# Kernel tuning notes

Measured on AMD Instinct MI355X. Metric: run time of the kernel, lower is better.

## Reference

```python
import jax, jax.numpy as jnp
import numpy as np

N = 50000          # nodes
E = 800000         # directed edges (avg degree 16)
D_IN = 128
H1, H2, H3 = 128, 128, 64


def setup_inputs() -> dict:
    key = jax.random.key(0)
    ks = jax.random.split(key, 12)
    s = 0.05  # small init scale
    return {
        "x": jax.random.normal(ks[0], (N, D_IN), dtype=jnp.float32),
        "edge_index": jax.random.randint(ks[1], (2, E), 0, N, dtype=jnp.int32),
        "W1": jax.random.normal(ks[2], (D_IN, H1), dtype=jnp.float32) * s,
        "b1": jnp.zeros((H1,), jnp.float32),
        "W2": jax.random.normal(ks[3], (H1, H2), dtype=jnp.float32) * s,
        "b2": jnp.zeros((H2,), jnp.float32),
        "W3": jax.random.normal(ks[4], (H2, H3), dtype=jnp.float32) * s,
        "b3": jnp.zeros((H3,), jnp.float32),
        "attn_W": jax.random.normal(ks[5], (H3, 1), dtype=jnp.float32) * s,
        "attn_b": jnp.zeros((1,), jnp.float32),
        "fc_W": jax.random.normal(ks[6], (H3, 1), dtype=jnp.float32) * s,
        "fc_b": jnp.zeros((1,), jnp.float32),
    }


def reference(x, edge_index, W1, b1, W2, b2, W3, b3, attn_W, attn_b, fc_W, fc_b):
    n = x.shape[0]
    self_loop = jnp.arange(n, dtype=edge_index.dtype)
    src = jnp.concatenate([edge_index[0], self_loop])  # [E+N]
    dst = jnp.concatenate([edge_index[1], self_loop])
    # GCN symmetric normalization with self-loops: deg over dst (col)
    deg = jax.ops.segment_sum(jnp.ones_like(dst, jnp.float32), dst, num_segments=n)
    dis = jax.lax.rsqrt(deg)  # deg >= 1 because of self-loops
    norm = dis[src] * dis[dst]  # [E+N]

    def gcn_conv(h, W, b):
        h = h @ W                                   # [N, out]
        msg = h[src] * norm[:, None]                # gather + scale
        out = jax.ops.segment_sum(msg, dst, num_segments=n)  # scatter-add
        return out + b

    h = jax.nn.relu(gcn_conv(x, W1, b1))
    # dropout: inference mode -> identity
    h = jax.nn.relu(gcn_conv(h, W2, b2))
    h = jax.nn.relu(gcn_conv(h, W3, b3))

    attn = jax.nn.softmax(h @ attn_W + attn_b, axis=0)  # softmax over node dim, [N,1]
    h = h * attn
    out = jax.nn.sigmoid(h @ fc_W + fc_b)  # [N,1]
    return out, attn
```

## Files before the change

kernel.cpp:

```cpp
#include <hip/hip_runtime.h>
#include <math.h>


typedef __attribute__((ext_vector_type(8))) short bf16x8;
typedef __attribute__((ext_vector_type(4))) float f32x4;

__device__ inline float bf2f(unsigned short u) {
  return __uint_as_float(((unsigned int)u) << 16);
}
__device__ inline unsigned short f2bf(float f) {
  unsigned int x = __float_as_uint(f);
  return (unsigned short)((x + 0x7FFFu + ((x >> 16) & 1u)) >> 16);
}
__device__ inline unsigned char f2fp8(float f) {
  int p = __builtin_amdgcn_cvt_pk_fp8_f32(f, f, 0, false);
  return (unsigned char)(p & 0xFF);
}

__global__ __launch_bounds__(256) void prep_kernel(int* __restrict__ counts,
    int* __restrict__ cursor, int n, const float* __restrict__ W1,
    const float* __restrict__ W2, const float* __restrict__ W3,
    unsigned short* __restrict__ Wt1, unsigned short* __restrict__ Wt2,
    unsigned short* __restrict__ Wt3) {
  int i = blockIdx.x * 256 + threadIdx.x;
  if (i < n) { counts[i] = 0; cursor[i] = 0; }
  if (i < 16384) {
    Wt1[(i & 127) * 128 + (i >> 7)] = f2bf(W1[i]);
  } else if (i < 32768) {
    int j = i - 16384;
    Wt2[(j & 127) * 128 + (j >> 7)] = f2bf(W2[j]);
  } else if (i < 40960) {
    int j = i - 32768;
    Wt3[(j & 63) * 128 + (j >> 6)] = f2bf(W3[j]);
  }
}

__global__ __launch_bounds__(256) void count_kernel(const int* __restrict__ dst,
                                                    int* __restrict__ counts, int E) {
  int e = blockIdx.x * blockDim.x + threadIdx.x;
  if (e < E) atomicAdd(&counts[dst[e]], 1);
}

__global__ __launch_bounds__(256) void block_sum_kernel(const int* __restrict__ counts,
                                                        int* __restrict__ bsums, int n) {
  int i = blockIdx.x * 256 + threadIdx.x;
  int v = (i < n) ? counts[i] : 0;
#pragma unroll
  for (int o = 32; o > 0; o >>= 1) v += __shfl_xor(v, o);
  __shared__ int w[4];
  if ((threadIdx.x & 63) == 0) w[threadIdx.x >> 6] = v;
  __syncthreads();
  if (threadIdx.x == 0) bsums[blockIdx.x] = w[0] + w[1] + w[2] + w[3];
}

__global__ __launch_bounds__(256) void block_scan_kernel(const int* __restrict__ bsums,
    int* __restrict__ bprefix, int* __restrict__ offsets, int nb, int n) {
  __shared__ int lds[256];
  int v = (threadIdx.x < (unsigned)nb) ? bsums[threadIdx.x] : 0;
  lds[threadIdx.x] = v;
  __syncthreads();
  for (int off = 1; off < 256; off <<= 1) {
    int t = (threadIdx.x >= (unsigned)off) ? lds[threadIdx.x - off] : 0;
    __syncthreads();
    lds[threadIdx.x] += t;
    __syncthreads();
  }
  if (threadIdx.x < (unsigned)nb) bprefix[threadIdx.x] = lds[threadIdx.x] - v;
  if (threadIdx.x == 255) offsets[n] = lds[255];
}

__global__ __launch_bounds__(256) void scan_apply_kernel(const int* __restrict__ counts,
    const int* __restrict__ bprefix, int* __restrict__ offsets,
    float* __restrict__ dis, int n) {
  __shared__ int lds[256];
  int i = blockIdx.x * 256 + threadIdx.x;
  int v = (i < n) ? counts[i] : 0;
  lds[threadIdx.x] = v;
  __syncthreads();
  for (int off = 1; off < 256; off <<= 1) {
    int t = (threadIdx.x >= (unsigned)off) ? lds[threadIdx.x - off] : 0;
    __syncthreads();
    lds[threadIdx.x] += t;
    __syncthreads();
  }
  if (i < n) {
    offsets[i] = bprefix[blockIdx.x] + lds[threadIdx.x] - v;
    dis[i] = rsqrtf((float)v + 1.0f);
  }
}

__global__ __launch_bounds__(256) void fill_kernel(const int* __restrict__ src,
    const int* __restrict__ dst, const int* __restrict__ offsets, int* __restrict__ cursor,
    const float* __restrict__ dis, unsigned int* __restrict__ csr, int E) {
  int e = blockIdx.x * blockDim.x + threadIdx.x;
  if (e >= E) return;
  int d = dst[e], s = src[e];
  int pos = offsets[d] + atomicAdd(&cursor[d], 1);
  csr[pos] = (unsigned int)s | ((unsigned int)f2bf(dis[s] * dis[d]) << 16);
}

template <int OUT, bool AF32>
__global__ __launch_bounds__(256) void gemm_mfma_kernel(const void* __restrict__ Ap,
    const unsigned short* __restrict__ Wt, unsigned char* __restrict__ T, int nrows) {
  constexpr int NC = OUT / 16;
  int wave = threadIdx.x >> 6;
  int lane = threadIdx.x & 63;
  int r15  = lane & 15;
  int kgrp = lane >> 4;
  int base = blockIdx.x * 64 + wave * 16;
  int row  = base + r15;

  f32x4 acc[NC];
#pragma unroll
  for (int c = 0; c < NC; c++) acc[c] = {0.f, 0.f, 0.f, 0.f};

#pragma unroll
  for (int kk = 0; kk < 4; kk++) {
    int k0 = kk * 32 + kgrp * 8;
    bf16x8 a = {0, 0, 0, 0, 0, 0, 0, 0};
    if (row < nrows) {
      if (AF32) {
        const float* A = (const float*)Ap;
        float4 lo = *(const float4*)(A + (size_t)row * 128 + k0);
        float4 hi = *(const float4*)(A + (size_t)row * 128 + k0 + 4);
        a[0] = (short)f2bf(lo.x); a[1] = (short)f2bf(lo.y);
        a[2] = (short)f2bf(lo.z); a[3] = (short)f2bf(lo.w);
        a[4] = (short)f2bf(hi.x); a[5] = (short)f2bf(hi.y);
        a[6] = (short)f2bf(hi.z); a[7] = (short)f2bf(hi.w);
      } else {
        const unsigned short* A = (const unsigned short*)Ap;
        a = *(const bf16x8*)(A + (size_t)row * 128 + k0);
      }
    }
#pragma unroll
    for (int c = 0; c < NC; c++) {
      bf16x8 b = *(const bf16x8*)(Wt + (size_t)(c * 16 + r15) * 128 + k0);
      acc[c] = __builtin_amdgcn_mfma_f32_16x16x32_bf16(a, b, acc[c], 0, 0, 0);
    }
  }

  int orow0 = base + kgrp * 4;
#pragma unroll
  for (int c = 0; c < NC; c++) {
#pragma unroll
    for (int j = 0; j < 4; j++) {
      int r = orow0 + j;
      if (r < nrows)
        T[(size_t)r * OUT + c * 16 + r15] = f2fp8(acc[c][j] * 16.f);
    }
  }
}

__global__ __launch_bounds__(256) void aggregate128_kernel(
    const unsigned char* __restrict__ T, const int* __restrict__ offsets,
    const unsigned int* __restrict__ csr, const float* __restrict__ dis,
    const float* __restrict__ bias, unsigned short* __restrict__ H, int n) {
  int node = (blockIdx.x * blockDim.x + threadIdx.x) >> 6;
  int lane = threadIdx.x & 63;
  if (node >= n) return;

  float di = dis[node];
  float sn = di * di;
  int beg = offsets[node], end = offsets[node + 1];

  unsigned int tv = *(const unsigned short*)(T + (size_t)node * 128 + lane * 2);
  float acc0 = __builtin_amdgcn_cvt_f32_fp8(tv, 0) * sn;
  float acc1 = __builtin_amdgcn_cvt_f32_fp8(tv, 1) * sn;

  int e = beg;
  for (; e + 8 <= end; e += 8) {
    uint4 q0 = *(const uint4*)(csr + e);
    uint4 q1 = *(const uint4*)(csr + e + 4);
    unsigned int t0 = *(const unsigned short*)(T + (size_t)(q0.x & 0xFFFF) * 128 + lane * 2);
    unsigned int t1 = *(const unsigned short*)(T + (size_t)(q0.y & 0xFFFF) * 128 + lane * 2);
    unsigned int t2 = *(const unsigned short*)(T + (size_t)(q0.z & 0xFFFF) * 128 + lane * 2);
    unsigned int t3 = *(const unsigned short*)(T + (size_t)(q0.w & 0xFFFF) * 128 + lane * 2);
    unsigned int t4 = *(const unsigned short*)(T + (size_t)(q1.x & 0xFFFF) * 128 + lane * 2);
    unsigned int t5 = *(const unsigned short*)(T + (size_t)(q1.y & 0xFFFF) * 128 + lane * 2);
    unsigned int t6 = *(const unsigned short*)(T + (size_t)(q1.z & 0xFFFF) * 128 + lane * 2);
    unsigned int t7 = *(const unsigned short*)(T + (size_t)(q1.w & 0xFFFF) * 128 + lane * 2);
    float n0 = bf2f((unsigned short)(q0.x >> 16));
    float n1 = bf2f((unsigned short)(q0.y >> 16));
    float n2 = bf2f((unsigned short)(q0.z >> 16));
    float n3 = bf2f((unsigned short)(q0.w >> 16));
    float n4 = bf2f((unsigned short)(q1.x >> 16));
    float n5 = bf2f((unsigned short)(q1.y >> 16));
    float n6 = bf2f((unsigned short)(q1.z >> 16));
    float n7 = bf2f((unsigned short)(q1.w >> 16));
    acc0 = fmaf(__builtin_amdgcn_cvt_f32_fp8(t0, 0), n0, acc0);
    acc1 = fmaf(__builtin_amdgcn_cvt_f32_fp8(t0, 1), n0, acc1);
    acc0 = fmaf(__builtin_amdgcn_cvt_f32_fp8(t1, 0), n1, acc0);
    acc1 = fmaf(__builtin_amdgcn_cvt_f32_fp8(t1, 1), n1, acc1);
    acc0 = fmaf(__builtin_amdgcn_cvt_f32_fp8(t2, 0), n2, acc0);
    acc1 = fmaf(__builtin_amdgcn_cvt_f32_fp8(t2, 1), n2, acc1);
    acc0 = fmaf(__builtin_amdgcn_cvt_f32_fp8(t3, 0), n3, acc0);
    acc1 = fmaf(__builtin_amdgcn_cvt_f32_fp8(t3, 1), n3, acc1);
    acc0 = fmaf(__builtin_amdgcn_cvt_f32_fp8(t4, 0), n4, acc0);
    acc1 = fmaf(__builtin_amdgcn_cvt_f32_fp8(t4, 1), n4, acc1);
    acc0 = fmaf(__builtin_amdgcn_cvt_f32_fp8(t5, 0), n5, acc0);
    acc1 = fmaf(__builtin_amdgcn_cvt_f32_fp8(t5, 1), n5, acc1);
    acc0 = fmaf(__builtin_amdgcn_cvt_f32_fp8(t6, 0), n6, acc0);
    acc1 = fmaf(__builtin_amdgcn_cvt_f32_fp8(t6, 1), n6, acc1);
    acc0 = fmaf(__builtin_amdgcn_cvt_f32_fp8(t7, 0), n7, acc0);
    acc1 = fmaf(__builtin_amdgcn_cvt_f32_fp8(t7, 1), n7, acc1);
  }
  for (; e < end; e++) {
    unsigned int c = csr[e];
    unsigned int tv2 = *(const unsigned short*)(T + (size_t)(c & 0xFFFF) * 128 + lane * 2);
    float nr = bf2f((unsigned short)(c >> 16));
    acc0 = fmaf(__builtin_amdgcn_cvt_f32_fp8(tv2, 0), nr, acc0);
    acc1 = fmaf(__builtin_amdgcn_cvt_f32_fp8(tv2, 1), nr, acc1);
  }
  float h0 = acc0 * 0.0625f + bias[lane * 2];
  float h1 = acc1 * 0.0625f + bias[lane * 2 + 1];
  ushort2 o;
  o.x = f2bf(h0 > 0.f ? h0 : 0.f);
  o.y = f2bf(h1 > 0.f ? h1 : 0.f);
  *(ushort2*)(H + (size_t)node * 128 + lane * 2) = o;
}

__global__ __launch_bounds__(256) void agg3_dots_kernel(
    const unsigned char* __restrict__ T, const int* __restrict__ offsets,
    const unsigned int* __restrict__ csr, const float* __restrict__ dis,
    const float* __restrict__ bias, const float* __restrict__ attn_W,
    const float* __restrict__ attn_b, const float* __restrict__ fc_W,
    float* __restrict__ logits, float* __restrict__ fdot, int n) {
  int node = (blockIdx.x * blockDim.x + threadIdx.x) >> 6;
  int lane = threadIdx.x & 63;
  if (node >= n) return;

  float di = dis[node];
  float sn = di * di;
  int beg = offsets[node], end = offsets[node + 1];

  unsigned int tv = T[(size_t)node * 64 + lane];
  float acc = __builtin_amdgcn_cvt_f32_fp8(tv, 0) * sn;

  int e = beg;
  for (; e + 8 <= end; e += 8) {
    uint4 q0 = *(const uint4*)(csr + e);
    uint4 q1 = *(const uint4*)(csr + e + 4);
    unsigned int t0 = T[(size_t)(q0.x & 0xFFFF) * 64 + lane];
    unsigned int t1 = T[(size_t)(q0.y & 0xFFFF) * 64 + lane];
    unsigned int t2 = T[(size_t)(q0.z & 0xFFFF) * 64 + lane];
    unsigned int t3 = T[(size_t)(q0.w & 0xFFFF) * 64 + lane];
    unsigned int t4 = T[(size_t)(q1.x & 0xFFFF) * 64 + lane];
    unsigned int t5 = T[(size_t)(q1.y & 0xFFFF) * 64 + lane];
    unsigned int t6 = T[(size_t)(q1.z & 0xFFFF) * 64 + lane];
    unsigned int t7 = T[(size_t)(q1.w & 0xFFFF) * 64 + lane];
    acc = fmaf(__builtin_amdgcn_cvt_f32_fp8(t0, 0), bf2f((unsigned short)(q0.x >> 16)), acc);
    acc = fmaf(__builtin_amdgcn_cvt_f32_fp8(t1, 0), bf2f((unsigned short)(q0.y >> 16)), acc);
    acc = fmaf(__builtin_amdgcn_cvt_f32_fp8(t2, 0), bf2f((unsigned short)(q0.z >> 16)), acc);
    acc = fmaf(__builtin_amdgcn_cvt_f32_fp8(t3, 0), bf2f((unsigned short)(q0.w >> 16)), acc);
    acc = fmaf(__builtin_amdgcn_cvt_f32_fp8(t4, 0), bf2f((unsigned short)(q1.x >> 16)), acc);
    acc = fmaf(__builtin_amdgcn_cvt_f32_fp8(t5, 0), bf2f((unsigned short)(q1.y >> 16)), acc);
    acc = fmaf(__builtin_amdgcn_cvt_f32_fp8(t6, 0), bf2f((unsigned short)(q1.z >> 16)), acc);
    acc = fmaf(__builtin_amdgcn_cvt_f32_fp8(t7, 0), bf2f((unsigned short)(q1.w >> 16)), acc);
  }
  for (; e < end; e++) {
    unsigned int c = csr[e];
    unsigned int tv2 = T[(size_t)(c & 0xFFFF) * 64 + lane];
    acc = fmaf(__builtin_amdgcn_cvt_f32_fp8(tv2, 0), bf2f((unsigned short)(c >> 16)), acc);
  }
  float h = acc * 0.0625f + bias[lane];
  h = h > 0.f ? h : 0.f;
  float a = h * attn_W[lane];
  float f = h * fc_W[lane];
#pragma unroll
  for (int m = 32; m > 0; m >>= 1) { a += __shfl_xor(a, m); f += __shfl_xor(f, m); }
  if (lane == 0) { logits[node] = a + attn_b[0]; fdot[node] = f; }
}

__global__ __launch_bounds__(256) void smax_partial_kernel(const float* __restrict__ l,
    float2* __restrict__ part, int n) {
  float m = -3.4e38f, s = 0.f;
  for (int i = blockIdx.x * 256 + threadIdx.x; i < n; i += gridDim.x * 256) {
    float v = l[i];
    float nm = fmaxf(m, v);
    s = s * __expf(m - nm) + __expf(v - nm);
    m = nm;
  }
#pragma unroll
  for (int o = 32; o > 0; o >>= 1) {
    float mo = __shfl_xor(m, o), so = __shfl_xor(s, o);
    float nm = fmaxf(m, mo);
    s = s * __expf(m - nm) + so * __expf(mo - nm);
    m = nm;
  }
  __shared__ float wm[4], ws[4];
  if ((threadIdx.x & 63) == 0) { wm[threadIdx.x >> 6] = m; ws[threadIdx.x >> 6] = s; }
  __syncthreads();
  if (threadIdx.x == 0) {
    float gm = fmaxf(fmaxf(wm[0], wm[1]), fmaxf(wm[2], wm[3]));
    float gs = ws[0] * __expf(wm[0] - gm) + ws[1] * __expf(wm[1] - gm) +
               ws[2] * __expf(wm[2] - gm) + ws[3] * __expf(wm[3] - gm);
    part[blockIdx.x] = make_float2(gm, gs);
  }
}

__global__ __launch_bounds__(64) void smax_combine_kernel(const float2* __restrict__ part,
    float2* __restrict__ gms, int np) {
  int lane = threadIdx.x;
  float m = -3.4e38f, s = 0.f;
  if (lane < np) { float2 p = part[lane]; m = p.x; s = p.y; }
#pragma unroll
  for (int o = 32; o > 0; o >>= 1) {
    float mo = __shfl_xor(m, o), so = __shfl_xor(s, o);
    float nm = fmaxf(m, mo);
    s = s * __expf(m - nm) + so * __expf(mo - nm);
    m = nm;
  }
  if (lane == 0) gms[0] = make_float2(m, s);
}

__global__ __launch_bounds__(256) void out_kernel(const float* __restrict__ l,
    const float2* __restrict__ gms, const float* __restrict__ fdot,
    const float* __restrict__ fc_b, float* __restrict__ out, int n) {
  int i = blockIdx.x * blockDim.x + threadIdx.x;
  if (i >= n) return;
  float2 g = gms[0];
  float attn = __expf(l[i] - g.x) / g.y;
  float z = fdot[i] * attn + fc_b[0];
  out[i]     = 1.f / (1.f + __expf(-z));
  out[n + i] = attn;
}

extern "C" void kernel_launch(void* const* d_in, const int* in_sizes, int n_in,
                              void* d_out, int out_size, void* d_ws, size_t ws_size,
                              hipStream_t stream) {
  const float* x      = (const float*)d_in[0];
  const int*   ei     = (const int*)d_in[1];
  const float* W1     = (const float*)d_in[2];
  const float* b1     = (const float*)d_in[3];
  const float* W2     = (const float*)d_in[4];
  const float* b2     = (const float*)d_in[5];
  const float* W3     = (const float*)d_in[6];
  const float* b3     = (const float*)d_in[7];
  const float* attn_W = (const float*)d_in[8];
  const float* attn_b = (const float*)d_in[9];
  const float* fc_W   = (const float*)d_in[10];
  const float* fc_b   = (const float*)d_in[11];

  const int N = in_sizes[0] / 128;
  const int E = in_sizes[1] / 2;
  const int NB = (N + 255) / 256;
  const int* src = ei;
  const int* dst = ei + E;

  char* p = (char*)d_ws;
  auto alloc = [&](size_t bytes) {
    void* r = (void*)p;
    p += (bytes + 255) & ~(size_t)255;
    return r;
  };
  int*   counts  = (int*)alloc((size_t)N * 4);
  int*   cursor  = (int*)alloc((size_t)N * 4);
  int*   offsets = (int*)alloc((size_t)(N + 1) * 4);
  float* dis     = (float*)alloc((size_t)N * 4);
  unsigned int*   csr  = (unsigned int*)alloc((size_t)E * 4);
  unsigned char*  tbuf = (unsigned char*)alloc((size_t)N * 128);
  unsigned short* hbuf = (unsigned short*)alloc((size_t)N * 128 * 2);
  unsigned short* wt1  = (unsigned short*)alloc(128 * 128 * 2);
  unsigned short* wt2  = (unsigned short*)alloc(128 * 128 * 2);
  unsigned short* wt3  = (unsigned short*)alloc(64 * 128 * 2);
  float* logits  = (float*)alloc((size_t)N * 4);
  float* fdot    = (float*)alloc((size_t)N * 4);
  int*   bsums   = (int*)alloc(256 * 4);
  int*   bprefix = (int*)alloc(256 * 4);
  float2* part   = (float2*)alloc(64 * 8);
  float2* gms    = (float2*)alloc(256);

  int PB = NB > 160 ? NB : 160;
  prep_kernel<<<PB, 256, 0, stream>>>(counts, cursor, N, W1, W2, W3, wt1, wt2, wt3);
  count_kernel<<<(E + 255) / 256, 256, 0, stream>>>(dst, counts, E);
  block_sum_kernel<<<NB, 256, 0, stream>>>(counts, bsums, N);
  block_scan_kernel<<<1, 256, 0, stream>>>(bsums, bprefix, offsets, NB, N);
  scan_apply_kernel<<<NB, 256, 0, stream>>>(counts, bprefix, offsets, dis, N);
  fill_kernel<<<(E + 255) / 256, 256, 0, stream>>>(src, dst, offsets, cursor, dis, csr, E);

  const int GB = (N + 63) / 64;
  gemm_mfma_kernel<128, true><<<GB, 256, 0, stream>>>(x, wt1, tbuf, N);
  aggregate128_kernel<<<(N + 3) / 4, 256, 0, stream>>>(tbuf, offsets, csr, dis, b1, hbuf, N);
  gemm_mfma_kernel<128, false><<<GB, 256, 0, stream>>>(hbuf, wt2, tbuf, N);
  aggregate128_kernel<<<(N + 3) / 4, 256, 0, stream>>>(tbuf, offsets, csr, dis, b2, hbuf, N);
  gemm_mfma_kernel<64, false><<<GB, 256, 0, stream>>>(hbuf, wt3, tbuf, N);
  agg3_dots_kernel<<<(N + 3) / 4, 256, 0, stream>>>(tbuf, offsets, csr, dis, b3,
                                                    attn_W, attn_b, fc_W, logits, fdot, N);

  smax_partial_kernel<<<64, 256, 0, stream>>>(logits, part, N);
  smax_combine_kernel<<<1, 64, 0, stream>>>(part, gms, 64);
  out_kernel<<<(N + 255) / 256, 256, 0, stream>>>(logits, gms, fdot, fc_b, (float*)d_out, N);
}
```

Baseline: 335.3 us.

## Split neighbor edges across sub-wave groups with 8-byte gathers; double GEMM rows per wave

The aggregation kernels now split each node's wavefront into sub-groups (4 for the 128-wide layers, 8 for the 64-wide layer). Each lane gathers 8 fp8 features with one 8-byte load, and different sub-groups handle different edges concurrently. Partial sums are then combined with cross-lane shuffles. This replaces narrow 1-2 byte per-lane gathers with wider loads and more independent memory requests in flight, at the cost of shuffle reductions and possibly idle sub-groups on low-degree nodes. Separately, the MFMA GEMM now computes 32 rows per wave instead of 16, which reuses each weight fragment load across two MFMAs at the cost of more registers.

After: 301.3 us. 10.2% less time.

```diff
diff --git a/kernel.cpp b/kernel.cpp
--- a/kernel.cpp
+++ b/kernel.cpp
@@ -4,6 +4,7 @@
 
 typedef __attribute__((ext_vector_type(8))) short bf16x8;
 typedef __attribute__((ext_vector_type(4))) float f32x4;
+typedef __attribute__((ext_vector_type(8))) unsigned short u16x8;
 
 __device__ inline float bf2f(unsigned short u) {
   return __uint_as_float(((unsigned int)u) << 16);
@@ -15,6 +16,26 @@
 __device__ inline unsigned char f2fp8(float f) {
   int p = __builtin_amdgcn_cvt_pk_fp8_f32(f, f, 0, false);
   return (unsigned char)(p & 0xFF);
+}
+__device__ inline void fp8x8_scale(uint2 t, float s, float (&acc)[8]) {
+  acc[0] = __builtin_amdgcn_cvt_f32_fp8(t.x, 0) * s;
+  acc[1] = __builtin_amdgcn_cvt_f32_fp8(t.x, 1) * s;
+  acc[2] = __builtin_amdgcn_cvt_f32_fp8(t.x, 2) * s;
+  acc[3] = __builtin_amdgcn_cvt_f32_fp8(t.x, 3) * s;
+  acc[4] = __builtin_amdgcn_cvt_f32_fp8(t.y, 0) * s;
+  acc[5] = __builtin_amdgcn_cvt_f32_fp8(t.y, 1) * s;
+  acc[6] = __builtin_amdgcn_cvt_f32_fp8(t.y, 2) * s;
+  acc[7] = __builtin_amdgcn_cvt_f32_fp8(t.y, 3) * s;
+}
+__device__ inline void fp8x8_fma(uint2 t, float nr, float (&acc)[8]) {
+  acc[0] = fmaf(__builtin_amdgcn_cvt_f32_fp8(t.x, 0), nr, acc[0]);
+  acc[1] = fmaf(__builtin_amdgcn_cvt_f32_fp8(t.x, 1), nr, acc[1]);
+  acc[2] = fmaf(__builtin_amdgcn_cvt_f32_fp8(t.x, 2), nr, acc[2]);
+  acc[3] = fmaf(__builtin_amdgcn_cvt_f32_fp8(t.x, 3), nr, acc[3]);
+  acc[4] = fmaf(__builtin_amdgcn_cvt_f32_fp8(t.y, 0), nr, acc[4]);
+  acc[5] = fmaf(__builtin_amdgcn_cvt_f32_fp8(t.y, 1), nr, acc[5]);
+  acc[6] = fmaf(__builtin_amdgcn_cvt_f32_fp8(t.y, 2), nr, acc[6]);
+  acc[7] = fmaf(__builtin_amdgcn_cvt_f32_fp8(t.y, 3), nr, acc[7]);
 }
 
 __global__ __launch_bounds__(256) void prep_kernel(int* __restrict__ counts,
@@ -107,46 +128,63 @@
   int lane = threadIdx.x & 63;
   int r15  = lane & 15;
   int kgrp = lane >> 4;
-  int base = blockIdx.x * 64 + wave * 16;
-  int row  = base + r15;
-
-  f32x4 acc[NC];
-#pragma unroll
-  for (int c = 0; c < NC; c++) acc[c] = {0.f, 0.f, 0.f, 0.f};
+  int base = blockIdx.x * 128 + wave * 32;
+  int row0 = base + r15;
+  int row1 = base + 16 + r15;
+
+  f32x4 acc[2][NC];
+#pragma unroll
+  for (int r = 0; r < 2; r++)
+#pragma unroll
+    for (int c = 0; c < NC; c++) acc[r][c] = {0.f, 0.f, 0.f, 0.f};
 
 #pragma unroll
   for (int kk = 0; kk < 4; kk++) {
     int k0 = kk * 32 + kgrp * 8;
-    bf16x8 a = {0, 0, 0, 0, 0, 0, 0, 0};
-    if (row < nrows) {
-      if (AF32) {
-        const float* A = (const float*)Ap;
-        float4 lo = *(const float4*)(A + (size_t)row * 128 + k0);
-        float4 hi = *(const float4*)(A + (size_t)row * 128 + k0 + 4);
-        a[0] = (short)f2bf(lo.x); a[1] = (short)f2bf(lo.y);
-        a[2] = (short)f2bf(lo.z); a[3] = (short)f2bf(lo.w);
-        a[4] = (short)f2bf(hi.x); a[5] = (short)f2bf(hi.y);
-        a[6] = (short)f2bf(hi.z); a[7] = (short)f2bf(hi.w);
-      } else {
-        const unsigned short* A = (const unsigned short*)Ap;
-        a = *(const bf16x8*)(A + (size_t)row * 128 + k0);
+    bf16x8 a0 = {0, 0, 0, 0, 0, 0, 0, 0};
+    bf16x8 a1 = {0, 0, 0, 0, 0, 0, 0, 0};
+    if (AF32) {
+      const float* A = (const float*)Ap;
+      if (row0 < nrows) {
+        float4 lo = *(const float4*)(A + (size_t)row0 * 128 + k0);
+        float4 hi = *(const float4*)(A + (size_t)row0 * 128 + k0 + 4);
+        a0[0] = (short)f2bf(lo.x); a0[1] = (short)f2bf(lo.y);
+        a0[2] = (short)f2bf(lo.z); a0[3] = (short)f2bf(lo.w);
+        a0[4] = (short)f2bf(hi.x); a0[5] = (short)f2bf(hi.y);
+        a0[6] = (short)f2bf(hi.z); a0[7] = (short)f2bf(hi.w);
       }
+      if (row1 < nrows) {
+        float4 lo = *(const float4*)(A + (size_t)row1 * 128 + k0);
+        float4 hi = *(const float4*)(A + (size_t)row1 * 128 + k0 + 4);
+        a1[0] = (short)f2bf(lo.x); a1[1] = (short)f2bf(lo.y);
+        a1[2] = (short)f2bf(lo.z); a1[3] = (short)f2bf(lo.w);
+        a1[4] = (short)f2bf(hi.x); a1[5] = (short)f2bf(hi.y);
+        a1[6] = (short)f2bf(hi.z); a1[7] = (short)f2bf(hi.w);
+      }
+    } else {
+      const unsigned short* A = (const unsigned short*)Ap;
+      if (row0 < nrows) a0 = *(const bf16x8*)(A + (size_t)row0 * 128 + k0);
+      if (row1 < nrows) a1 = *(const bf16x8*)(A + (size_t)row1 * 128 + k0);
     }
 #pragma unroll
     for (int c = 0; c < NC; c++) {
       bf16x8 b = *(const bf16x8*)(Wt + (size_t)(c * 16 + r15) * 128 + k0);
-      acc[c] = __builtin_amdgcn_mfma_f32_16x16x32_bf16(a, b, acc[c], 0, 0, 0);
+      acc[0][c] = __builtin_amdgcn_mfma_f32_16x16x32_bf16(a0, b, acc[0][c], 0, 0, 0);
+      acc[1][c] = __builtin_amdgcn_mfma_f32_16x16x32_bf16(a1, b, acc[1][c], 0, 0, 0);
     }
   }
 
-  int orow0 = base + kgrp * 4;
-#pragma unroll
-  for (int c = 0; c < NC; c++) {
-#pragma unroll
-    for (int j = 0; j < 4; j++) {
-      int r = orow0 + j;
-      if (r < nrows)
-        T[(size_t)r * OUT + c * 16 + r15] = f2fp8(acc[c][j] * 16.f);
+#pragma unroll
+  for (int r = 0; r < 2; r++) {
+    int orow0 = base + r * 16 + kgrp * 4;
+#pragma unroll
+    for (int c = 0; c < NC; c++) {
+#pragma unroll
+      for (int j = 0; j < 4; j++) {
+        int rr = orow0 + j;
+        if (rr < nrows)
+          T[(size_t)rr * OUT + c * 16 + r15] = f2fp8(acc[r][c][j] * 16.f);
+      }
     }
   }
 }
@@ -158,65 +196,52 @@
   int node = (blockIdx.x * blockDim.x + threadIdx.x) >> 6;
   int lane = threadIdx.x & 63;
   if (node >= n) return;
+  int sub = lane >> 4;
+  int fl  = lane & 15;
 
   float di = dis[node];
   float sn = di * di;
   int beg = offsets[node], end = offsets[node + 1];
 
-  unsigned int tv = *(const unsigned short*)(T + (size_t)node * 128 + lane * 2);
-  float acc0 = __builtin_amdgcn_cvt_f32_fp8(tv, 0) * sn;
-  float acc1 = __builtin_amdgcn_cvt_f32_fp8(tv, 1) * sn;
-
-  int e = beg;
-  for (; e + 8 <= end; e += 8) {
-    uint4 q0 = *(const uint4*)(csr + e);
-    uint4 q1 = *(const uint4*)(csr + e + 4);
-    unsigned int t0 = *(const unsigned short*)(T + (size_t)(q0.x & 0xFFFF) * 128 + lane * 2);
-    unsigned int t1 = *(const unsigned short*)(T + (size_t)(q0.y & 0xFFFF) * 128 + lane * 2);
-    unsigned int t2 = *(const unsigned short*)(T + (size_t)(q0.z & 0xFFFF) * 128 + lane * 2);
-    unsigned int t3 = *(const unsigned short*)(T + (size_t)(q0.w & 0xFFFF) * 128 + lane * 2);
-    unsigned int t4 = *(const unsigned short*)(T + (size_t)(q1.x & 0xFFFF) * 128 + lane * 2);
-    unsigned int t5 = *(const unsigned short*)(T + (size_t)(q1.y & 0xFFFF) * 128 + lane * 2);
-    unsigned int t6 = *(const unsigned short*)(T + (size_t)(q1.z & 0xFFFF) * 128 + lane * 2);
-    unsigned int t7 = *(const unsigned short*)(T + (size_t)(q1.w & 0xFFFF) * 128 + lane * 2);
-    float n0 = bf2f((unsigned short)(q0.x >> 16));
-    float n1 = bf2f((unsigned short)(q0.y >> 16));
-    float n2 = bf2f((unsigned short)(q0.z >> 16));
-    float n3 = bf2f((unsigned short)(q0.w >> 16));
-    float n4 = bf2f((unsigned short)(q1.x >> 16));
-    float n5 = bf2f((unsigned short)(q1.y >> 16));
-    float n6 = bf2f((unsigned short)(q1.z >> 16));
-    float n7 = bf2f((unsigned short)(q1.w >> 16));
-    acc0 = fmaf(__builtin_amdgcn_cvt_f32_fp8(t0, 0), n0, acc0);
-    acc1 = fmaf(__builtin_amdgcn_cvt_f32_fp8(t0, 1), n0, acc1);
-    acc0 = fmaf(__builtin_amdgcn_cvt_f32_fp8(t1, 0), n1, acc0);
-    acc1 = fmaf(__builtin_amdgcn_cvt_f32_fp8(t1, 1), n1, acc1);
-    acc0 = fmaf(__builtin_amdgcn_cvt_f32_fp8(t2, 0), n2, acc0);
-    acc1 = fmaf(__builtin_amdgcn_cvt_f32_fp8(t2, 1), n2, acc1);
-    acc0 = fmaf(__builtin_amdgcn_cvt_f32_fp8(t3, 0), n3, acc0);
-    acc1 = fmaf(__builtin_amdgcn_cvt_f32_fp8(t3, 1), n3, acc1);
-    acc0 = fmaf(__builtin_amdgcn_cvt_f32_fp8(t4, 0), n4, acc0);
-    acc1 = fmaf(__builtin_amdgcn_cvt_f32_fp8(t4, 1), n4, acc1);
-    acc0 = fmaf(__builtin_amdgcn_cvt_f32_fp8(t5, 0), n5, acc0);
-    acc1 = fmaf(__builtin_amdgcn_cvt_f32_fp8(t5, 1), n5, acc1);
-    acc0 = fmaf(__builtin_amdgcn_cvt_f32_fp8(t6, 0), n6, acc0);
-    acc1 = fmaf(__builtin_amdgcn_cvt_f32_fp8(t6, 1), n6, acc1);
-    acc0 = fmaf(__builtin_amdgcn_cvt_f32_fp8(t7, 0), n7, acc0);
-    acc1 = fmaf(__builtin_amdgcn_cvt_f32_fp8(t7, 1), n7, acc1);
-  }
-  for (; e < end; e++) {
-    unsigned int c = csr[e];
-    unsigned int tv2 = *(const unsigned short*)(T + (size_t)(c & 0xFFFF) * 128 + lane * 2);
-    float nr = bf2f((unsigned short)(c >> 16));
-    acc0 = fmaf(__builtin_amdgcn_cvt_f32_fp8(tv2, 0), nr, acc0);
-    acc1 = fmaf(__builtin_amdgcn_cvt_f32_fp8(tv2, 1), nr, acc1);
-  }
-  float h0 = acc0 * 0.0625f + bias[lane * 2];
-  float h1 = acc1 * 0.0625f + bias[lane * 2 + 1];
-  ushort2 o;
-  o.x = f2bf(h0 > 0.f ? h0 : 0.f);
-  o.y = f2bf(h1 > 0.f ? h1 : 0.f);
-  *(ushort2*)(H + (size_t)node * 128 + lane * 2) = o;
+  float acc[8];
+  {
+    uint2 tv = *(const uint2*)(T + (size_t)node * 128 + fl * 8);
+    fp8x8_scale(tv, (sub == 0) ? sn : 0.f, acc);
+  }
+
+  int e = beg + sub;
+  for (; e + 4 < end; e += 8) {
+    unsigned int c0 = csr[e], c1 = csr[e + 4];
+    uint2 t0 = *(const uint2*)(T + (size_t)(c0 & 0xFFFF) * 128 + fl * 8);
+    uint2 t1 = *(const uint2*)(T + (size_t)(c1 & 0xFFFF) * 128 + fl * 8);
+    fp8x8_fma(t0, bf2f((unsigned short)(c0 >> 16)), acc);
+    fp8x8_fma(t1, bf2f((unsigned short)(c1 >> 16)), acc);
+  }
+  if (e < end) {
+    unsigned int c0 = csr[e];
+    uint2 t0 = *(const uint2*)(T + (size_t)(c0 & 0xFFFF) * 128 + fl * 8);
+    fp8x8_fma(t0, bf2f((unsigned short)(c0 >> 16)), acc);
+  }
+
+#pragma unroll
+  for (int j = 0; j < 8; j++) {
+    acc[j] += __shfl_xor(acc[j], 16);
+    acc[j] += __shfl_xor(acc[j], 32);
+  }
+
+  if (sub == 0) {
+    float4 b0 = *(const float4*)(bias + fl * 8);
+    float4 b1 = *(const float4*)(bias + fl * 8 + 4);
+    float hb[8];
+    hb[0] = acc[0] * 0.0625f + b0.x; hb[1] = acc[1] * 0.0625f + b0.y;
+    hb[2] = acc[2] * 0.0625f + b0.z; hb[3] = acc[3] * 0.0625f + b0.w;
+    hb[4] = acc[4] * 0.0625f + b1.x; hb[5] = acc[5] * 0.0625f + b1.y;
+    hb[6] = acc[6] * 0.0625f + b1.z; hb[7] = acc[7] * 0.0625f + b1.w;
+    u16x8 o;
+#pragma unroll
+    for (int j = 0; j < 8; j++) o[j] = f2bf(hb[j] > 0.f ? hb[j] : 0.f);
+    *(u16x8*)(H + (size_t)node * 128 + fl * 8) = o;
+  }
 }
 
 __global__ __launch_bounds__(256) void agg3_dots_kernel(
@@ -228,46 +253,59 @@
   int node = (blockIdx.x * blockDim.x + threadIdx.x) >> 6;
   int lane = threadIdx.x & 63;
   if (node >= n) return;
+  int sub = lane >> 3;
+  int fl  = lane & 7;
 
   float di = dis[node];
   float sn = di * di;
   int beg = offsets[node], end = offsets[node + 1];
 
-  unsigned int tv = T[(size_t)node * 64 + lane];
-  float acc = __builtin_amdgcn_cvt_f32_fp8(tv, 0) * sn;
-
-  int e = beg;
-  for (; e + 8 <= end; e += 8) {
-    uint4 q0 = *(const uint4*)(csr + e);
-    uint4 q1 = *(const uint4*)(csr + e + 4);
-    unsigned int t0 = T[(size_t)(q0.x & 0xFFFF) * 64 + lane];
-    unsigned int t1 = T[(size_t)(q0.y & 0xFFFF) * 64 + lane];
-    unsigned int t2 = T[(size_t)(q0.z & 0xFFFF) * 64 + lane];
-    unsigned int t3 = T[(size_t)(q0.w & 0xFFFF) * 64 + lane];
-    unsigned int t4 = T[(size_t)(q1.x & 0xFFFF) * 64 + lane];
-    unsigned int t5 = T[(size_t)(q1.y & 0xFFFF) * 64 + lane];
-    unsigned int t6 = T[(size_t)(q1.z & 0xFFFF) * 64 + lane];
-    unsigned int t7 = T[(size_t)(q1.w & 0xFFFF) * 64 + lane];
-    acc = fmaf(__builtin_amdgcn_cvt_f32_fp8(t0, 0), bf2f((unsigned short)(q0.x >> 16)), acc);
-    acc = fmaf(__builtin_amdgcn_cvt_f32_fp8(t1, 0), bf2f((unsigned short)(q0.y >> 16)), acc);
-    acc = fmaf(__builtin_amdgcn_cvt_f32_fp8(t2, 0), bf2f((unsigned short)(q0.z >> 16)), acc);
-    acc = fmaf(__builtin_amdgcn_cvt_f32_fp8(t3, 0), bf2f((unsigned short)(q0.w >> 16)), acc);
-    acc = fmaf(__builtin_amdgcn_cvt_f32_fp8(t4, 0), bf2f((unsigned short)(q1.x >> 16)), acc);
-    acc = fmaf(__builtin_amdgcn_cvt_f32_fp8(t5, 0), bf2f((unsigned short)(q1.y >> 16)), acc);
-    acc = fmaf(__builtin_amdgcn_cvt_f32_fp8(t6, 0), bf2f((unsigned short)(q1.z >> 16)), acc);
-    acc = fmaf(__builtin_amdgcn_cvt_f32_fp8(t7, 0), bf2f((unsigned short)(q1.w >> 16)), acc);
-  }
-  for (; e < end; e++) {
-    unsigned int c = csr[e];
-    unsigned int tv2 = T[(size_t)(c & 0xFFFF) * 64 + lane];
-    acc = fmaf(__builtin_amdgcn_cvt_f32_fp8(tv2, 0), bf2f((unsigned short)(c >> 16)), acc);
-  }
-  float h = acc * 0.0625f + bias[lane];
-  h = h > 0.f ? h : 0.f;
-  float a = h * attn_W[lane];
-  float f = h * fc_W[lane];
-#pragma unroll
-  for (int m = 32; m > 0; m >>= 1) { a += __shfl_xor(a, m); f += __shfl_xor(f, m); }
+  float acc[8];
+  {
+    uint2 tv = *(const uint2*)(T + (size_t)node * 64 + fl * 8);
+    fp8x8_scale(tv, (sub == 0) ? sn : 0.f, acc);
+  }
+
+  int e = beg + sub;
+  for (; e + 8 < end; e += 16) {
+    unsigned int c0 = csr[e], c1 = csr[e + 8];
+    uint2 t0 = *(const uint2*)(T + (size_t)(c0 & 0xFFFF) * 64 + fl * 8);
+    uint2 t1 = *(const uint2*)(T + (size_t)(c1 & 0xFFFF) * 64 + fl * 8);
+    fp8x8_fma(t0, bf2f((unsigned short)(c0 >> 16)), acc);
+    fp8x8_fma(t1, bf2f((unsigned short)(c1 >> 16)), acc);
+  }
+  if (e < end) {
+    unsigned int c0 = csr[e];
+    uint2 t0 = *(const uint2*)(T + (size_t)(c0 & 0xFFFF) * 64 + fl * 8);
+    fp8x8_fma(t0, bf2f((unsigned short)(c0 >> 16)), acc);
+  }
+
+#pragma unroll
+  for (int j = 0; j < 8; j++) {
+    acc[j] += __shfl_xor(acc[j], 8);
+    acc[j] += __shfl_xor(acc[j], 16);
+    acc[j] += __shfl_xor(acc[j], 32);
+  }
+
+  float4 b0 = *(const float4*)(bias + fl * 8);
+  float4 b1 = *(const float4*)(bias + fl * 8 + 4);
+  float4 aw0 = *(const float4*)(attn_W + fl * 8);
+  float4 aw1 = *(const float4*)(attn_W + fl * 8 + 4);
+  float4 fw0 = *(const float4*)(fc_W + fl * 8);
+  float4 fw1 = *(const float4*)(fc_W + fl * 8 + 4);
+  float h[8];
+  h[0] = acc[0] * 0.0625f + b0.x; h[1] = acc[1] * 0.0625f + b0.y;
+  h[2] = acc[2] * 0.0625f + b0.z; h[3] = acc[3] * 0.0625f + b0.w;
+  h[4] = acc[4] * 0.0625f + b1.x; h[5] = acc[5] * 0.0625f + b1.y;
+  h[6] = acc[6] * 0.0625f + b1.z; h[7] = acc[7] * 0.0625f + b1.w;
+#pragma unroll
+  for (int j = 0; j < 8; j++) h[j] = h[j] > 0.f ? h[j] : 0.f;
+  float a = h[0] * aw0.x + h[1] * aw0.y + h[2] * aw0.z + h[3] * aw0.w +
+            h[4] * aw1.x + h[5] * aw1.y + h[6] * aw1.z + h[7] * aw1.w;
+  float f = h[0] * fw0.x + h[1] * fw0.y + h[2] * fw0.z + h[3] * fw0.w +
+            h[4] * fw1.x + h[5] * fw1.y + h[6] * fw1.z + h[7] * fw1.w;
+#pragma unroll
+  for (int m = 4; m > 0; m >>= 1) { a += __shfl_xor(a, m); f += __shfl_xor(f, m); }
   if (lane == 0) { logits[node] = a + attn_b[0]; fdot[node] = f; }
 }
 
@@ -378,7 +416,7 @@
   scan_apply_kernel<<<NB, 256, 0, stream>>>(counts, bprefix, offsets, dis, N);
   fill_kernel<<<(E + 255) / 256, 256, 0, stream>>>(src, dst, offsets, cursor, dis, csr, E);
 
-  const int GB = (N + 63) / 64;
+  const int GB = (N + 127) / 128;
   gemm_mfma_kernel<128, true><<<GB, 256, 0, stream>>>(x, wt1, tbuf, N);
   aggregate128_kernel<<<(N + 3) / 4, 256, 0, stream>>>(tbuf, offsets, csr, dis, b1, hbuf, N);
   gemm_mfma_kernel<128, false><<<GB, 256, 0, stream>>>(hbuf, wt2, tbuf, N);
```
